# Performance work log

Measured on AMD Instinct MI355X. Metric: run time of the kernel, lower is better.

## Reference

```python
import jax, jax.numpy as jnp
import numpy as np

B, T, H = 4096, 2048, 64


def setup_inputs() -> dict:
    key = jax.random.key(0)
    ks = jax.random.split(key, 8)
    inp = {
        "returns": jax.random.normal(ks[0], (B, T, 1), jnp.float32) * 0.1,
        "log_rv": jax.random.normal(ks[1], (B, T, 1), jnp.float32) * 0.5,
        # scalar GARCH parameters (shape [1], matching nn.Parameter(torch.tensor([v])))
        "omega": jnp.array([0.01], jnp.float32),
        "beta": jnp.array([0.8], jnp.float32),
        "tau1": jnp.array([0.1], jnp.float32),
        "tau2": jnp.array([0.1], jnp.float32),
        "gamma": jnp.array([0.1], jnp.float32),
        "xi": jnp.array([0.0], jnp.float32),
        "phi": jnp.array([1.0], jnp.float32),
        "delta1": jnp.array([0.1], jnp.float32),
        "delta2": jnp.array([0.1], jnp.float32),
        "mu": jnp.array([0.0], jnp.float32),
        # MLP enhancement: Linear(3,H) -> ReLU -> Linear(H,H) -> ReLU -> Linear(H,1)
        "W1": jax.random.normal(ks[2], (3, H), jnp.float32) / np.float32(np.sqrt(3.0)),
        "b1": jnp.zeros((H,), jnp.float32),
        "W2": jax.random.normal(ks[3], (H, H), jnp.float32) / np.float32(np.sqrt(H)),
        "b2": jnp.zeros((H,), jnp.float32),
        "W3": jax.random.normal(ks[4], (H, 1), jnp.float32) / np.float32(np.sqrt(H)),
        "b3": jnp.zeros((1,), jnp.float32),
    }
    return inp


def _forward(returns, log_rv, omega, beta, tau1, tau2, gamma, xi, phi,
             delta1, delta2, mu, W1, b1, W2, b2, W3, b3):
    def mlp(x):  # x: [B, 3]
        h = jax.nn.relu(x @ W1 + b1)
        h = jax.nn.relu(h @ W2 + b2)
        return h @ W3 + b3  # [B, 1]

    def measure(log_h_t, r_t, lrv_t):
        # log_h_t, r_t, lrv_t: [B, 1]
        h_t = jnp.exp(log_h_t)
        z_t = (r_t - mu) / jnp.sqrt(h_t)
        delta_t = delta1 * z_t + delta2 * (z_t ** 2 - 1.0)
        u_t = lrv_t - (xi + phi * log_h_t + delta_t)
        log_x_t = xi + phi * log_h_t + delta_t + u_t
        nn_out = mlp(jnp.concatenate([log_h_t, z_t, u_t], axis=-1))
        enhanced = log_h_t + 0.01 * nn_out  # stored & carried value
        return enhanced, log_x_t, z_t, u_t

    rs = jnp.swapaxes(returns, 0, 1)   # [T, B, 1]
    lrvs = jnp.swapaxes(log_rv, 0, 1)  # [T, B, 1]

    # t = 0: h_prev = mean(exp(log_rv[:, 0:1, :]), dim=1) == exp(log_rv[:, 0, :])
    log_h0 = jnp.log(jnp.mean(jnp.exp(lrvs[0:1]), axis=0))  # [B, 1]
    enh0, lx0, z0, u0 = measure(log_h0, rs[0], lrvs[0])

    def step(carry, xs):
        lh_prev, z_prev, u_prev = carry  # previous (enhanced) log_h, z, u
        r_t, lrv_t = xs
        log_h_t = (omega + beta * lh_prev
                   + tau1 * z_prev + tau2 * (z_prev ** 2 - 1.0)
                   + gamma * u_prev)
        enh, lx, z_t, u_t = measure(log_h_t, r_t, lrv_t)
        return (enh, z_t, u_t), (enh, lx, z_t, u_t)

    _, (lh_r, lx_r, z_r, u_r) = jax.lax.scan(step, (enh0, z0, u0), (rs[1:], lrvs[1:]))

    def assemble(first, rest):  # [B,1] + [T-1,B,1] -> [B,T,1]
        return jnp.swapaxes(jnp.concatenate([first[None], rest], axis=0), 0, 1)

    return (assemble(enh0, lh_r), assemble(lx0, lx_r),
            assemble(z0, z_r), assemble(u0, u_r))


def reference(returns, log_rv, omega, beta, tau1, tau2, gamma, xi, phi,
              delta1, delta2, mu, W1, b1, W2, b2, W3, b3):
    return _forward(returns, log_rv, omega, beta, tau1, tau2, gamma, xi, phi,
                    delta1, delta2, mu, W1, b1, W2, b2, W3, b3)
```

## Files before the change

### kernel.cpp

```cpp
#include <hip/hip_runtime.h>


constexpr int Bn  = 4096;
constexpr int Tn  = 2048;
constexpr int SEG = 256;
constexpr int WU  = 64;
constexpr int CH  = 32;

typedef _Float16 h2v   __attribute__((ext_vector_type(2)));
typedef _Float16 f16x4 __attribute__((ext_vector_type(4)));
typedef _Float16 f16x8 __attribute__((ext_vector_type(8)));
typedef float    f32x4 __attribute__((ext_vector_type(4)));

__global__ __launch_bounds__(64, 2)
void garch_scan_kernel(const float* __restrict__ g_ret,
                       const float* __restrict__ g_lrv,
                       const float* __restrict__ p_omega,
                       const float* __restrict__ p_beta,
                       const float* __restrict__ p_tau1,
                       const float* __restrict__ p_tau2,
                       const float* __restrict__ p_gamma,
                       const float* __restrict__ p_xi,
                       const float* __restrict__ p_phi,
                       const float* __restrict__ p_delta1,
                       const float* __restrict__ p_delta2,
                       const float* __restrict__ p_mu,
                       const float* __restrict__ W1,
                       const float* __restrict__ b1,
                       const float* __restrict__ W2,
                       const float* __restrict__ b2,
                       const float* __restrict__ W3,
                       const float* __restrict__ b3,
                       float* __restrict__ out)
{
    const int l = threadIdx.x;
    const int c = l & 15;
    const int g = l >> 4;
    const int bid = blockIdx.x;
    const int seg = bid >> 8;
    const long cb = (long)(bid & 255) * 16;

    const int t_start = seg ? seg * SEG - WU : 0;
    const int nsteps  = seg ? SEG + WU : SEG;
    const int nwu     = seg ? WU : 0;

    const float omega = p_omega[0], beta = p_beta[0];
    const float tau1 = p_tau1[0], tau2 = p_tau2[0], gam = p_gamma[0];
    const float xi = p_xi[0], phi = p_phi[0];
    const float d1 = p_delta1[0], d2 = p_delta2[0], mu = p_mu[0];
    const float b3s = b3[0];

    h2v w1xp[8], w1yp[8], w1zp[8], b1p[8];
#pragma unroll
    for (int q = 0; q < 8; ++q) {
        const int kt = q >> 2, jp = q & 3;
        const int k0 = 32 * kt + 8 * g + 2 * jp;
        h2v a;
        a.x = (_Float16)W1[k0];        a.y = (_Float16)W1[k0 + 1];        w1xp[q] = a;
        a.x = (_Float16)W1[64 + k0];   a.y = (_Float16)W1[64 + k0 + 1];   w1yp[q] = a;
        a.x = (_Float16)W1[128 + k0];  a.y = (_Float16)W1[128 + k0 + 1];  w1zp[q] = a;
        a.x = (_Float16)b1[k0];        a.y = (_Float16)b1[k0 + 1];        b1p[q] = a;
    }

    f16x8 aw2[2][4];
#pragma unroll
    for (int kt = 0; kt < 2; ++kt)
#pragma unroll
        for (int mt = 0; mt < 4; ++mt)
#pragma unroll
            for (int j = 0; j < 8; ++j)
                aw2[kt][mt][j] = (_Float16)W2[(32 * kt + 8 * g + j) * 64 + 16 * mt + c];

    f32x4 binit[4];
#pragma unroll
    for (int mt = 0; mt < 4; ++mt)
#pragma unroll
        for (int i = 0; i < 4; ++i)
            binit[mt][i] = b2[16 * mt + 4 * g + i];

    h2v w3pk[4][2];
#pragma unroll
    for (int mt = 0; mt < 4; ++mt) {
        h2v a;
        a.x = (_Float16)W3[16 * mt + 4 * g + 0];
        a.y = (_Float16)W3[16 * mt + 4 * g + 1];
        w3pk[mt][0] = a;
        a.x = (_Float16)W3[16 * mt + 4 * g + 2];
        a.y = (_Float16)W3[16 * mt + 4 * g + 3];
        w3pk[mt][1] = a;
    }

    __shared__ __align__(16) float2 lds_in[16][36];
    __shared__ __align__(16) float2 ldsA[16][36];
    __shared__ __align__(16) float2 ldsB[16][36];

    const float* rbase = g_ret + cb * Tn;
    const float* lbase = g_lrv + cb * Tn;
    const float2* pin = &lds_in[c][0];
    float2* pA = &ldsA[c][0];
    float2* pB = &ldsB[c][0];

    float lh = 0.0f, zp = 0.0f, z2m1 = -1.0f, up = 0.0f;
    const h2v hzero = {(_Float16)0.0f, (_Float16)0.0f};

    for (int tc = 0; tc < nsteps; tc += CH) {
        {
            const int ss = l & 31, chf = l >> 5;
#pragma unroll
            for (int k = 0; k < 8; ++k) {
                const int ch = 2 * k + chf;
                const long base = (long)ch * Tn + t_start + tc + ss;
                lds_in[ch][ss] = make_float2(rbase[base], lbase[base]);
            }
        }
        asm volatile("" ::: "memory");

#pragma unroll 4
        for (int tw = 0; tw < CH; ++tw) {
            const float2 rl = pin[tw];
            const float r_t = rl.x, lrv_t = rl.y;

            const float sA = fmaf(beta, lh, omega);
            const float sB = fmaf(tau2, z2m1, tau1 * zp);
            const float sC = fmaf(gam, up, sA + sB);
            const float lh_t = (tc == 0 && tw == 0) ? lrv_t : sC;

            const float z_t  = (r_t - mu) * __expf(-0.5f * lh_t);
            const float z2n  = fmaf(z_t, z_t, -1.0f);
            const float dlt  = fmaf(d2, z2n, d1 * z_t);
            const float a_t  = fmaf(phi, lh_t, xi) + dlt;
            const float u_t  = lrv_t - a_t;
            const float lx_t = a_t + u_t;

            const h2v lh2 = __builtin_bit_cast(h2v, __builtin_amdgcn_cvt_pkrtz(lh_t, lh_t));
            const h2v zz2 = __builtin_bit_cast(h2v, __builtin_amdgcn_cvt_pkrtz(z_t,  z_t));
            const h2v uu2 = __builtin_bit_cast(h2v, __builtin_amdgcn_cvt_pkrtz(u_t,  u_t));

            h2v q[8];
#pragma unroll
            for (int p = 0; p < 8; ++p) {
                h2v h = __builtin_elementwise_fma(w1xp[p], lh2, b1p[p]);
                h = __builtin_elementwise_fma(w1yp[p], zz2, h);
                h = __builtin_elementwise_fma(w1zp[p], uu2, h);
                q[p] = __builtin_elementwise_max(h, hzero);
            }
            const f16x4 lo0 = __builtin_shufflevector(q[0], q[1], 0, 1, 2, 3);
            const f16x4 hi0 = __builtin_shufflevector(q[2], q[3], 0, 1, 2, 3);
            const f16x8 bf0 = __builtin_shufflevector(lo0, hi0, 0, 1, 2, 3, 4, 5, 6, 7);
            const f16x4 lo1 = __builtin_shufflevector(q[4], q[5], 0, 1, 2, 3);
            const f16x4 hi1 = __builtin_shufflevector(q[6], q[7], 0, 1, 2, 3);
            const f16x8 bf1 = __builtin_shufflevector(lo1, hi1, 0, 1, 2, 3, 4, 5, 6, 7);

            f32x4 acc[4];
#pragma unroll
            for (int mt = 0; mt < 4; ++mt) {
                f32x4 t4 = __builtin_amdgcn_mfma_f32_16x16x32_f16(aw2[0][mt], bf0, binit[mt], 0, 0, 0);
                acc[mt]  = __builtin_amdgcn_mfma_f32_16x16x32_f16(aw2[1][mt], bf1, t4, 0, 0, 0);
            }

            float dA = 0.0f, dB = 0.0f;
#pragma unroll
            for (int mt = 0; mt < 4; ++mt) {
                h2v p01 = __builtin_bit_cast(h2v, __builtin_amdgcn_cvt_pkrtz(acc[mt][0], acc[mt][1]));
                h2v p23 = __builtin_bit_cast(h2v, __builtin_amdgcn_cvt_pkrtz(acc[mt][2], acc[mt][3]));
                p01 = __builtin_elementwise_max(p01, hzero);
                p23 = __builtin_elementwise_max(p23, hzero);
                if (mt < 2) {
                    dA = __builtin_amdgcn_fdot2(p01, w3pk[mt][0], dA, false);
                    dA = __builtin_amdgcn_fdot2(p23, w3pk[mt][1], dA, false);
                } else {
                    dB = __builtin_amdgcn_fdot2(p01, w3pk[mt][0], dB, false);
                    dB = __builtin_amdgcn_fdot2(p23, w3pk[mt][1], dB, false);
                }
            }
            const float part = dA + dB;

            const float s16 = part + __builtin_bit_cast(float,
                __builtin_amdgcn_ds_swizzle(__builtin_bit_cast(int, part), 0x401F));
            float nns;
#if __has_builtin(__builtin_amdgcn_permlane32_swap)
            {
                auto r2 = __builtin_amdgcn_permlane32_swap(
                    __builtin_bit_cast(unsigned int, s16),
                    __builtin_bit_cast(unsigned int, s16), false, false);
                nns = __builtin_bit_cast(float, (unsigned int)r2[0])
                    + __builtin_bit_cast(float, (unsigned int)r2[1]);
            }
#else
            nns = s16 + __shfl_xor(s16, 32, 64);
#endif
            const float nn  = nns + b3s;
            const float enh = fmaf(0.01f, nn, lh_t);
            if (l < 16) {
                pA[tw] = make_float2(enh, lx_t);
                pB[tw] = make_float2(z_t, u_t);
            }
            lh = enh; zp = z_t; z2m1 = z2n; up = u_t;
        }

        asm volatile("" ::: "memory");

        if (tc >= nwu) {
            const int  cd = l >> 2, tb = l & 3;
            const long chd = cb + cd;
            const int  ta = t_start + tc + 8 * tb;
            float* oLH = out + 0l * Bn * Tn + chd * Tn + ta;
            float* oLX = out + 1l * Bn * Tn + chd * Tn + ta;
            float* oZ  = out + 2l * Bn * Tn + chd * Tn + ta;
            float* oU  = out + 3l * Bn * Tn + chd * Tn + ta;
#pragma unroll
            for (int i = 0; i < 2; ++i) {
                const float4 pA01 = *(const float4*)&ldsA[cd][8 * tb + 4 * i];
                const float4 pA23 = *(const float4*)&ldsA[cd][8 * tb + 4 * i + 2];
                const float4 pB01 = *(const float4*)&ldsB[cd][8 * tb + 4 * i];
                const float4 pB23 = *(const float4*)&ldsB[cd][8 * tb + 4 * i + 2];
                *(float4*)&oLH[4 * i] = make_float4(pA01.x, pA01.z, pA23.x, pA23.z);
                *(float4*)&oLX[4 * i] = make_float4(pA01.y, pA01.w, pA23.y, pA23.w);
                *(float4*)&oZ [4 * i] = make_float4(pB01.x, pB01.z, pB23.x, pB23.z);
                *(float4*)&oU [4 * i] = make_float4(pB01.y, pB01.w, pB23.y, pB23.w);
            }
        }
        asm volatile("" ::: "memory");
    }
}

extern "C" void kernel_launch(void* const* d_in, const int* in_sizes, int n_in,
                              void* d_out, int out_size, void* d_ws, size_t ws_size,
                              hipStream_t stream) {
    const float* g_ret = (const float*)d_in[0];
    const float* g_lrv = (const float*)d_in[1];
    const float* p_omega  = (const float*)d_in[2];
    const float* p_beta   = (const float*)d_in[3];
    const float* p_tau1   = (const float*)d_in[4];
    const float* p_tau2   = (const float*)d_in[5];
    const float* p_gamma  = (const float*)d_in[6];
    const float* p_xi     = (const float*)d_in[7];
    const float* p_phi    = (const float*)d_in[8];
    const float* p_delta1 = (const float*)d_in[9];
    const float* p_delta2 = (const float*)d_in[10];
    const float* p_mu     = (const float*)d_in[11];
    const float* W1 = (const float*)d_in[12];
    const float* b1 = (const float*)d_in[13];
    const float* W2 = (const float*)d_in[14];
    const float* b2 = (const float*)d_in[15];
    const float* W3 = (const float*)d_in[16];
    const float* b3 = (const float*)d_in[17];
    float* out = (float*)d_out;

    dim3 grid((Tn / SEG) * (Bn / 16)), block(64);
    hipLaunchKernelGGL(garch_scan_kernel, grid, block, 0, stream,
                       g_ret, g_lrv, p_omega, p_beta, p_tau1, p_tau2, p_gamma,
                       p_xi, p_phi, p_delta1, p_delta2, p_mu,
                       W1, b1, W2, b2, W3, b3, out);
}
```

Baseline: 161.5 us.

## Switch to 32x32x16 MFMA covering 32 chains per wave with shorter segments

Each wave now runs 32 batch chains instead of 16. The hidden-layer matmul moves from 16x16x32 to 32x32x16 MFMA, with W1/W2/W3 fragments and the reduction rebuilt for the new layout. The time segment shrinks to 128 steps with a 32-step warm-up, which halves the serial step count per wave while keeping the grid size unchanged. In exchange each step carries a longer dependent MFMA chain and higher register use. The shorter warm-up may also reduce accuracy at segment boundaries.

```diff
diff --git a/kernel.cpp b/kernel.cpp
--- a/kernel.cpp
+++ b/kernel.cpp
@@ -3,16 +3,23 @@
 
 constexpr int Bn  = 4096;
 constexpr int Tn  = 2048;
-constexpr int SEG = 256;
-constexpr int WU  = 64;
-constexpr int CH  = 32;
-
-typedef _Float16 h2v   __attribute__((ext_vector_type(2)));
-typedef _Float16 f16x4 __attribute__((ext_vector_type(4)));
-typedef _Float16 f16x8 __attribute__((ext_vector_type(8)));
-typedef float    f32x4 __attribute__((ext_vector_type(4)));
-
-__global__ __launch_bounds__(64, 2)
+constexpr int SEG = 128;
+constexpr int WU  = 32;
+constexpr int CH  = 16;
+
+typedef _Float16 h2v    __attribute__((ext_vector_type(2)));
+typedef _Float16 f16x8  __attribute__((ext_vector_type(8)));
+typedef float    f32x16 __attribute__((ext_vector_type(16)));
+typedef unsigned int u32x4 __attribute__((ext_vector_type(4)));
+
+__device__ __forceinline__ f16x8 splat8(float v) {
+    const unsigned int u = __builtin_bit_cast(unsigned int,
+        __builtin_amdgcn_cvt_pkrtz(v, v));
+    u32x4 t = {u, u, u, u};
+    return __builtin_bit_cast(f16x8, t);
+}
+
+__global__ __launch_bounds__(64, 1)
 void garch_scan_kernel(const float* __restrict__ g_ret,
                        const float* __restrict__ g_lrv,
                        const float* __restrict__ p_omega,
@@ -33,12 +40,12 @@
                        const float* __restrict__ b3,
                        float* __restrict__ out)
 {
-    const int l = threadIdx.x;
-    const int c = l & 15;
-    const int g = l >> 4;
+    const int l  = threadIdx.x;
+    const int ch = l & 31;
+    const int hi = l >> 5;
     const int bid = blockIdx.x;
-    const int seg = bid >> 8;
-    const long cb = (long)(bid & 255) * 16;
+    const int seg = bid >> 7;
+    const long cb = (long)(bid & 127) * 32;
 
     const int t_start = seg ? seg * SEG - WU : 0;
     const int nsteps  = seg ? SEG + WU : SEG;
@@ -50,67 +57,65 @@
     const float d1 = p_delta1[0], d2 = p_delta2[0], mu = p_mu[0];
     const float b3s = b3[0];
 
-    h2v w1xp[8], w1yp[8], w1zp[8], b1p[8];
-#pragma unroll
-    for (int q = 0; q < 8; ++q) {
-        const int kt = q >> 2, jp = q & 3;
-        const int k0 = 32 * kt + 8 * g + 2 * jp;
-        h2v a;
-        a.x = (_Float16)W1[k0];        a.y = (_Float16)W1[k0 + 1];        w1xp[q] = a;
-        a.x = (_Float16)W1[64 + k0];   a.y = (_Float16)W1[64 + k0 + 1];   w1yp[q] = a;
-        a.x = (_Float16)W1[128 + k0];  a.y = (_Float16)W1[128 + k0 + 1];  w1zp[q] = a;
-        a.x = (_Float16)b1[k0];        a.y = (_Float16)b1[k0 + 1];        b1p[q] = a;
-    }
-
-    f16x8 aw2[2][4];
-#pragma unroll
-    for (int kt = 0; kt < 2; ++kt)
-#pragma unroll
-        for (int mt = 0; mt < 4; ++mt)
+    f16x8 w1x8[4], w1y8[4], w1z8[4], b18[4];
+#pragma unroll
+    for (int kt = 0; kt < 4; ++kt)
+#pragma unroll
+        for (int j = 0; j < 8; ++j) {
+            const int kk = 16 * kt + 8 * hi + j;
+            w1x8[kt][j] = (_Float16)W1[kk];
+            w1y8[kt][j] = (_Float16)W1[64 + kk];
+            w1z8[kt][j] = (_Float16)W1[128 + kk];
+            b18[kt][j]  = (_Float16)b1[kk];
+        }
+
+    f16x8 aw2[4][2];
+#pragma unroll
+    for (int kt = 0; kt < 4; ++kt)
+#pragma unroll
+        for (int mt = 0; mt < 2; ++mt)
 #pragma unroll
             for (int j = 0; j < 8; ++j)
-                aw2[kt][mt][j] = (_Float16)W2[(32 * kt + 8 * g + j) * 64 + 16 * mt + c];
-
-    f32x4 binit[4];
-#pragma unroll
-    for (int mt = 0; mt < 4; ++mt)
-#pragma unroll
-        for (int i = 0; i < 4; ++i)
-            binit[mt][i] = b2[16 * mt + 4 * g + i];
-
-    h2v w3pk[4][2];
-#pragma unroll
-    for (int mt = 0; mt < 4; ++mt) {
-        h2v a;
-        a.x = (_Float16)W3[16 * mt + 4 * g + 0];
-        a.y = (_Float16)W3[16 * mt + 4 * g + 1];
-        w3pk[mt][0] = a;
-        a.x = (_Float16)W3[16 * mt + 4 * g + 2];
-        a.y = (_Float16)W3[16 * mt + 4 * g + 3];
-        w3pk[mt][1] = a;
-    }
-
-    __shared__ __align__(16) float2 lds_in[16][36];
-    __shared__ __align__(16) float2 ldsA[16][36];
-    __shared__ __align__(16) float2 ldsB[16][36];
+                aw2[kt][mt][j] = (_Float16)W2[(16 * kt + 8 * hi + j) * 64 + 32 * mt + ch];
+
+    f32x16 binit[2];
+#pragma unroll
+    for (int mt = 0; mt < 2; ++mt)
+#pragma unroll
+        for (int r = 0; r < 16; ++r)
+            binit[mt][r] = b2[(r & 3) + 8 * (r >> 2) + 4 * hi + 32 * mt];
+
+    h2v w3pk[2][8];
+#pragma unroll
+    for (int mt = 0; mt < 2; ++mt)
+#pragma unroll
+        for (int i = 0; i < 8; ++i) {
+            const int row = ((2 * i) & 3) + 8 * (i >> 1) + 4 * hi + 32 * mt;
+            h2v a; a.x = (_Float16)W3[row]; a.y = (_Float16)W3[row + 1];
+            w3pk[mt][i] = a;
+        }
+
+    __shared__ __align__(16) float2 lds_in[32][17];
+    __shared__ __align__(16) float2 ldsA[32][17];
+    __shared__ __align__(16) float2 ldsB[32][17];
 
     const float* rbase = g_ret + cb * Tn;
     const float* lbase = g_lrv + cb * Tn;
-    const float2* pin = &lds_in[c][0];
-    float2* pA = &ldsA[c][0];
-    float2* pB = &ldsB[c][0];
+    const float2* pin = &lds_in[ch][0];
+    float2* pA = &ldsA[ch][0];
+    float2* pB = &ldsB[ch][0];
 
     float lh = 0.0f, zp = 0.0f, z2m1 = -1.0f, up = 0.0f;
-    const h2v hzero = {(_Float16)0.0f, (_Float16)0.0f};
+    const f16x8 zero8 = {};
 
     for (int tc = 0; tc < nsteps; tc += CH) {
         {
-            const int ss = l & 31, chf = l >> 5;
+            const int ss = l & 15, chq = l >> 4;
 #pragma unroll
             for (int k = 0; k < 8; ++k) {
-                const int ch = 2 * k + chf;
-                const long base = (long)ch * Tn + t_start + tc + ss;
-                lds_in[ch][ss] = make_float2(rbase[base], lbase[base]);
+                const int cc = 4 * k + chq;
+                const long base = (long)cc * Tn + t_start + tc + ss;
+                lds_in[cc][ss] = make_float2(rbase[base], lbase[base]);
             }
         }
         asm volatile("" ::: "memory");
@@ -132,66 +137,57 @@
             const float u_t  = lrv_t - a_t;
             const float lx_t = a_t + u_t;
 
-            const h2v lh2 = __builtin_bit_cast(h2v, __builtin_amdgcn_cvt_pkrtz(lh_t, lh_t));
-            const h2v zz2 = __builtin_bit_cast(h2v, __builtin_amdgcn_cvt_pkrtz(z_t,  z_t));
-            const h2v uu2 = __builtin_bit_cast(h2v, __builtin_amdgcn_cvt_pkrtz(u_t,  u_t));
-
-            h2v q[8];
-#pragma unroll
-            for (int p = 0; p < 8; ++p) {
-                h2v h = __builtin_elementwise_fma(w1xp[p], lh2, b1p[p]);
-                h = __builtin_elementwise_fma(w1yp[p], zz2, h);
-                h = __builtin_elementwise_fma(w1zp[p], uu2, h);
-                q[p] = __builtin_elementwise_max(h, hzero);
-            }
-            const f16x4 lo0 = __builtin_shufflevector(q[0], q[1], 0, 1, 2, 3);
-            const f16x4 hi0 = __builtin_shufflevector(q[2], q[3], 0, 1, 2, 3);
-            const f16x8 bf0 = __builtin_shufflevector(lo0, hi0, 0, 1, 2, 3, 4, 5, 6, 7);
-            const f16x4 lo1 = __builtin_shufflevector(q[4], q[5], 0, 1, 2, 3);
-            const f16x4 hi1 = __builtin_shufflevector(q[6], q[7], 0, 1, 2, 3);
-            const f16x8 bf1 = __builtin_shufflevector(lo1, hi1, 0, 1, 2, 3, 4, 5, 6, 7);
-
-            f32x4 acc[4];
-#pragma unroll
-            for (int mt = 0; mt < 4; ++mt) {
-                f32x4 t4 = __builtin_amdgcn_mfma_f32_16x16x32_f16(aw2[0][mt], bf0, binit[mt], 0, 0, 0);
-                acc[mt]  = __builtin_amdgcn_mfma_f32_16x16x32_f16(aw2[1][mt], bf1, t4, 0, 0, 0);
+            const f16x8 lh8 = splat8(lh_t);
+            const f16x8 zz8 = splat8(z_t);
+            const f16x8 uu8 = splat8(u_t);
+
+            f16x8 bfr[4];
+#pragma unroll
+            for (int kt = 0; kt < 4; ++kt) {
+                f16x8 h = __builtin_elementwise_fma(w1x8[kt], lh8, b18[kt]);
+                h = __builtin_elementwise_fma(w1y8[kt], zz8, h);
+                h = __builtin_elementwise_fma(w1z8[kt], uu8, h);
+                bfr[kt] = __builtin_elementwise_max(h, zero8);
+            }
+
+            f32x16 acc[2];
+#pragma unroll
+            for (int mt = 0; mt < 2; ++mt) {
+                f32x16 a = __builtin_amdgcn_mfma_f32_32x32x16_f16(aw2[0][mt], bfr[0], binit[mt], 0, 0, 0);
+                a = __builtin_amdgcn_mfma_f32_32x32x16_f16(aw2[1][mt], bfr[1], a, 0, 0, 0);
+                a = __builtin_amdgcn_mfma_f32_32x32x16_f16(aw2[2][mt], bfr[2], a, 0, 0, 0);
+                acc[mt] = __builtin_amdgcn_mfma_f32_32x32x16_f16(aw2[3][mt], bfr[3], a, 0, 0, 0);
             }
 
             float dA = 0.0f, dB = 0.0f;
-#pragma unroll
-            for (int mt = 0; mt < 4; ++mt) {
-                h2v p01 = __builtin_bit_cast(h2v, __builtin_amdgcn_cvt_pkrtz(acc[mt][0], acc[mt][1]));
-                h2v p23 = __builtin_bit_cast(h2v, __builtin_amdgcn_cvt_pkrtz(acc[mt][2], acc[mt][3]));
-                p01 = __builtin_elementwise_max(p01, hzero);
-                p23 = __builtin_elementwise_max(p23, hzero);
-                if (mt < 2) {
-                    dA = __builtin_amdgcn_fdot2(p01, w3pk[mt][0], dA, false);
-                    dA = __builtin_amdgcn_fdot2(p23, w3pk[mt][1], dA, false);
-                } else {
-                    dB = __builtin_amdgcn_fdot2(p01, w3pk[mt][0], dB, false);
-                    dB = __builtin_amdgcn_fdot2(p23, w3pk[mt][1], dB, false);
+            const h2v hz2 = {(_Float16)0.0f, (_Float16)0.0f};
+#pragma unroll
+            for (int mt = 0; mt < 2; ++mt)
+#pragma unroll
+                for (int i = 0; i < 8; ++i) {
+                    h2v p = __builtin_bit_cast(h2v,
+                        __builtin_amdgcn_cvt_pkrtz(acc[mt][2 * i], acc[mt][2 * i + 1]));
+                    p = __builtin_elementwise_max(p, hz2);
+                    if (i & 1) dB = __builtin_amdgcn_fdot2(p, w3pk[mt][i], dB, false);
+                    else       dA = __builtin_amdgcn_fdot2(p, w3pk[mt][i], dA, false);
                 }
-            }
             const float part = dA + dB;
 
-            const float s16 = part + __builtin_bit_cast(float,
-                __builtin_amdgcn_ds_swizzle(__builtin_bit_cast(int, part), 0x401F));
             float nns;
 #if __has_builtin(__builtin_amdgcn_permlane32_swap)
             {
                 auto r2 = __builtin_amdgcn_permlane32_swap(
-                    __builtin_bit_cast(unsigned int, s16),
-                    __builtin_bit_cast(unsigned int, s16), false, false);
+                    __builtin_bit_cast(unsigned int, part),
+                    __builtin_bit_cast(unsigned int, part), false, false);
                 nns = __builtin_bit_cast(float, (unsigned int)r2[0])
                     + __builtin_bit_cast(float, (unsigned int)r2[1]);
             }
 #else
-            nns = s16 + __shfl_xor(s16, 32, 64);
+            nns = part + __shfl_xor(part, 32, 64);
 #endif
             const float nn  = nns + b3s;
             const float enh = fmaf(0.01f, nn, lh_t);
-            if (l < 16) {
+            if (l < 32) {
                 pA[tw] = make_float2(enh, lx_t);
                 pB[tw] = make_float2(z_t, u_t);
             }
@@ -201,19 +197,20 @@
         asm volatile("" ::: "memory");
 
         if (tc >= nwu) {
-            const int  cd = l >> 2, tb = l & 3;
+            const int  cd = l >> 1, th = l & 1;
             const long chd = cb + cd;
-            const int  ta = t_start + tc + 8 * tb;
+            const int  ta = t_start + tc + 8 * th;
             float* oLH = out + 0l * Bn * Tn + chd * Tn + ta;
             float* oLX = out + 1l * Bn * Tn + chd * Tn + ta;
             float* oZ  = out + 2l * Bn * Tn + chd * Tn + ta;
             float* oU  = out + 3l * Bn * Tn + chd * Tn + ta;
 #pragma unroll
             for (int i = 0; i < 2; ++i) {
-                const float4 pA01 = *(const float4*)&ldsA[cd][8 * tb + 4 * i];
-                const float4 pA23 = *(const float4*)&ldsA[cd][8 * tb + 4 * i + 2];
-                const float4 pB01 = *(const float4*)&ldsB[cd][8 * tb + 4 * i];
-                const float4 pB23 = *(const float4*)&ldsB[cd][8 * tb + 4 * i + 2];
+                const int s0 = 8 * th + 4 * i;
+                const float4 pA01 = *(const float4*)&ldsA[cd][s0];
+                const float4 pA23 = *(const float4*)&ldsA[cd][s0 + 2];
+                const float4 pB01 = *(const float4*)&ldsB[cd][s0];
+                const float4 pB23 = *(const float4*)&ldsB[cd][s0 + 2];
                 *(float4*)&oLH[4 * i] = make_float4(pA01.x, pA01.z, pA23.x, pA23.z);
                 *(float4*)&oLX[4 * i] = make_float4(pA01.y, pA01.w, pA23.y, pA23.w);
                 *(float4*)&oZ [4 * i] = make_float4(pB01.x, pB01.z, pB23.x, pB23.z);
@@ -247,7 +244,7 @@
     const float* b3 = (const float*)d_in[17];
     float* out = (float*)d_out;
 
-    dim3 grid((Tn / SEG) * (Bn / 16)), block(64);
+    dim3 grid((Tn / SEG) * (Bn / 32)), block(64);
     hipLaunchKernelGGL(garch_scan_kernel, grid, block, 0, stream,
                        g_ret, g_lrv, p_omega, p_beta, p_tau1, p_tau2, p_gamma,
                        p_xi, p_phi, p_delta1, p_delta2, p_mu,
```

Result: slower. 186.8 us (+15.7%).
